# Optimization experiments

Measured on AMD Instinct MI355X. Metric: run time of the kernel, lower is better.

The kernel has to match this reference:

```python
import jax, jax.numpy as jnp
import numpy as np

N_HEAD = 16
N_KV_HEAD = 4
HEAD_DIM = 64  # n_embd // n_head = 1024 // 16
N_EMBD = 1024


def _alibi_bias(T, n_head, head_dim):
    # slopes: start = 2**(-2**(-(log2(H)-3))); slope_i = start**(i+1)
    start = 2.0 ** (-2.0 ** (-(np.log2(n_head) - 3.0)))
    slopes = jnp.asarray(start ** np.arange(1, n_head + 1), dtype=jnp.float32)  # [H]
    rel = (jnp.arange(T, dtype=jnp.float32)[None, :]
           - jnp.arange(T, dtype=jnp.float32)[:, None])  # [T,T], rel[i,j] = j - i
    bias = slopes[:, None, None] * rel[None, :, :]  # [H,T,T]
    # Faithful to the torch module: masked_fill(-inf) is then OVERWRITTEN by
    # torch.tril, which zeroes the upper triangle. Net effect: lower-tri alibi
    # values, 0 above the diagonal (NO causal masking).
    bias = jnp.tril(bias)
    return bias * (head_dim ** -0.5)  # extra scale applied in forward


def setup_inputs() -> dict:
    key = jax.random.key(0)
    ks = jax.random.split(key, 5)
    B, T, C = 4, 2048, N_EMBD
    w_scale = 0.02
    return {
        "x": jax.random.normal(ks[0], (B, T, C), dtype=jnp.float32),
        "Wq": jax.random.normal(ks[1], (C, C), dtype=jnp.float32) * w_scale,
        "Wkv": jax.random.normal(ks[2], (2 * N_KV_HEAD * HEAD_DIM, C), dtype=jnp.float32) * w_scale,
        "Wproj": jax.random.normal(ks[3], (C, C), dtype=jnp.float32) * w_scale,
        "bproj": jnp.zeros((C,), dtype=jnp.float32),
    }


def reference(x, Wq, Wkv, Wproj, bproj):
    B, T, C = x.shape
    H, KVH, D = N_HEAD, N_KV_HEAD, HEAD_DIM
    ratio = H // KVH

    q = jnp.einsum('btc,ec->bte', x, Wq).reshape(B, T, H, D).transpose(0, 2, 1, 3)  # [B,H,T,D]
    kv = jnp.einsum('btc,ec->bte', x, Wkv)  # [B,T,2*KVH*D]
    k, v = jnp.split(kv, 2, axis=-1)
    k = k.reshape(B, T, KVH, D).transpose(0, 2, 1, 3)  # [B,KVH,T,D]
    v = v.reshape(B, T, KVH, D).transpose(0, 2, 1, 3)
    # torch .repeat tiles whole blocks: query head h uses kv head h % KVH
    k = jnp.tile(k, (1, ratio, 1, 1))  # [B,H,T,D]
    v = jnp.tile(v, (1, ratio, 1, 1))

    bias = _alibi_bias(T, H, D)  # [H,T,T], already *= D**-0.5
    scores = jnp.einsum('bhtd,bhsd->bhts', q, k) * (D ** -0.5) + bias[None]
    attn = jax.nn.softmax(scores, axis=-1)
    out = jnp.einsum('bhts,bhsd->bhtd', attn, v)  # [B,H,T,D]
    out = out.transpose(0, 2, 1, 3).reshape(B, T, C)
    return jnp.einsum('btc,ec->bte', out, Wproj) + bproj
```

## Files before the change

### kernel.cpp

```cpp
#include <hip/hip_runtime.h>
#include <hip/hip_bf16.h>
#include <cstdint>

typedef __bf16 bf16;
typedef bf16 bf16x2 __attribute__((ext_vector_type(2)));
typedef bf16 bf16x4 __attribute__((ext_vector_type(4)));
typedef bf16 bf16x8 __attribute__((ext_vector_type(8)));
typedef float f32x4 __attribute__((ext_vector_type(4)));
typedef unsigned int uint32x2_t __attribute__((ext_vector_type(2)));
typedef unsigned int uint32x4_t __attribute__((ext_vector_type(4)));

#define MFMA16(a, b, c) __builtin_amdgcn_mfma_f32_16x16x32_bf16((a), (b), (c), 0, 0, 0)

#define QSCALE 0.18033688011112042f

__device__ inline void async16(const bf16* g, bf16* l) {
  __builtin_amdgcn_global_load_lds(
      (const __attribute__((address_space(1))) void*)g,
      (__attribute__((address_space(3))) void*)l, 16, 0, 0);
}

__global__ void cast_all(const float* __restrict__ x, const float* __restrict__ wq,
                         const float* __restrict__ wkv, const float* __restrict__ wp,
                         bf16* __restrict__ xb, bf16* __restrict__ w1b,
                         bf16* __restrict__ wpb) {
  const int i = blockIdx.x * blockDim.x + threadIdx.x;
  const float4* src;
  bf16x4* dst;
  int idx;
  if (i < 2097152) {
    src = (const float4*)x; dst = (bf16x4*)xb; idx = i;
  } else if (i < 2359296) {
    src = (const float4*)wq; dst = (bf16x4*)w1b; idx = i - 2097152;
  } else if (i < 2490368) {
    src = (const float4*)wkv; dst = (bf16x4*)(w1b + 1048576); idx = i - 2359296;
  } else {
    src = (const float4*)wp; dst = (bf16x4*)wpb; idx = i - 2490368;
  }
  const float4 v = src[idx];
  bf16x4 o;
  o.x = (bf16)v.x; o.y = (bf16)v.y; o.z = (bf16)v.z; o.w = (bf16)v.w;
  dst[idx] = o;
}

__global__ __launch_bounds__(256, 2)
void gemm_qkv(const bf16* __restrict__ A, const bf16* __restrict__ B,
              bf16* __restrict__ qb, bf16* __restrict__ kb, bf16* __restrict__ vb) {
  constexpr int K = 1024;
  __shared__ bf16 sA[128 * 64];
  __shared__ bf16 sB[128 * 64];
  const int tid = threadIdx.x;
  const int lane = tid & 63, wid = tid >> 6;
  const int col = lane & 15, quad = lane >> 4;
  const int wm = wid >> 1, wn = wid & 1;
  const int m0 = blockIdx.y * 128, n0 = blockIdx.x * 128;
  const int c7 = col & 7;

  f32x4 acc[4][4];
  const f32x4 z = {0.f, 0.f, 0.f, 0.f};
#pragma unroll
  for (int mi = 0; mi < 4; mi++)
#pragma unroll
    for (int ni = 0; ni < 4; ni++) acc[mi][ni] = z;

  for (int k0 = 0; k0 < K; k0 += 64) {
    __syncthreads();
#pragma unroll
    for (int c = 0; c < 4; ++c) {
      const int idx = c * 256 + tid;
      const int row = idx >> 3, kc = idx & 7;
      const int gkc = kc ^ (row & 7);
      async16(&A[(size_t)(m0 + row) * K + k0 + gkc * 8], &sA[idx * 8]);
      async16(&B[(size_t)(n0 + row) * K + k0 + gkc * 8], &sB[idx * 8]);
    }
    __syncthreads();
#pragma unroll
    for (int ks = 0; ks < 2; ++ks) {
      bf16x8 af[4], bfr[4];
#pragma unroll
      for (int i = 0; i < 4; i++)
        af[i] = *(const bf16x8*)&sA[(wm * 64 + i * 16 + col) * 64 +
                                    (((ks * 4 + quad) ^ c7) << 3)];
#pragma unroll
      for (int i = 0; i < 4; i++)
        bfr[i] = *(const bf16x8*)&sB[(wn * 64 + i * 16 + col) * 64 +
                                     (((ks * 4 + quad) ^ c7) << 3)];
#pragma unroll
      for (int mi = 0; mi < 4; mi++)
#pragma unroll
        for (int ni = 0; ni < 4; ni++)
          acc[mi][ni] = MFMA16(af[mi], bfr[ni], acc[mi][ni]);
    }
  }
#pragma unroll
  for (int mi = 0; mi < 4; mi++) {
#pragma unroll
    for (int ni = 0; ni < 4; ni++) {
      const int e = n0 + wn * 64 + ni * 16 + col;
#pragma unroll
      for (int r = 0; r < 4; r++) {
        const int m = m0 + wm * 64 + mi * 16 + quad * 4 + r;
        const int bb = m >> 11, t = m & 2047;
        if (e < 1024) {
          qb[(((size_t)bb * 16 + (e >> 6)) * 2048 + t) * 64 + (e & 63)] =
              (bf16)(acc[mi][ni][r] * QSCALE);
        } else if (e < 1280) {
          const int f = e - 1024;
          kb[(((size_t)bb * 4 + (f >> 6)) * 2048 + t) * 64 + (f & 63)] =
              (bf16)acc[mi][ni][r];
        } else {
          const int f = e - 1280;
          vb[(((size_t)bb * 4 + (f >> 6)) * 2048 + t) * 64 + (f & 63)] =
              (bf16)acc[mi][ni][r];
        }
      }
    }
  }
}

__global__ __launch_bounds__(256, 2)
void gemm_proj(const bf16* __restrict__ A, const bf16* __restrict__ B,
               const float* __restrict__ bias, float* __restrict__ out) {
  constexpr int K = 1024;
  __shared__ bf16 sA[128 * 64];
  __shared__ bf16 sB[128 * 64];
  const int tid = threadIdx.x;
  const int lane = tid & 63, wid = tid >> 6;
  const int col = lane & 15, quad = lane >> 4;
  const int wm = wid >> 1, wn = wid & 1;
  const int m0 = blockIdx.y * 128, n0 = blockIdx.x * 128;
  const int c7 = col & 7;

  f32x4 acc[4][4];
  const f32x4 z = {0.f, 0.f, 0.f, 0.f};
#pragma unroll
  for (int mi = 0; mi < 4; mi++)
#pragma unroll
    for (int ni = 0; ni < 4; ni++) acc[mi][ni] = z;

  for (int k0 = 0; k0 < K; k0 += 64) {
    __syncthreads();
#pragma unroll
    for (int c = 0; c < 4; ++c) {
      const int idx = c * 256 + tid;
      const int row = idx >> 3, kc = idx & 7;
      const int gkc = kc ^ (row & 7);
      async16(&A[(size_t)(m0 + row) * K + k0 + gkc * 8], &sA[idx * 8]);
      async16(&B[(size_t)(n0 + row) * K + k0 + gkc * 8], &sB[idx * 8]);
    }
    __syncthreads();
#pragma unroll
    for (int ks = 0; ks < 2; ++ks) {
      bf16x8 af[4], bfr[4];
#pragma unroll
      for (int i = 0; i < 4; i++)
        af[i] = *(const bf16x8*)&sA[(wm * 64 + i * 16 + col) * 64 +
                                    (((ks * 4 + quad) ^ c7) << 3)];
#pragma unroll
      for (int i = 0; i < 4; i++)
        bfr[i] = *(const bf16x8*)&sB[(wn * 64 + i * 16 + col) * 64 +
                                     (((ks * 4 + quad) ^ c7) << 3)];
#pragma unroll
      for (int mi = 0; mi < 4; mi++)
#pragma unroll
        for (int ni = 0; ni < 4; ni++)
          acc[mi][ni] = MFMA16(af[mi], bfr[ni], acc[mi][ni]);
    }
  }
#pragma unroll
  for (int mi = 0; mi < 4; mi++) {
#pragma unroll
    for (int ni = 0; ni < 4; ni++) {
      const int e = n0 + wn * 64 + ni * 16 + col;
      const float be = bias[e];
#pragma unroll
      for (int r = 0; r < 4; r++) {
        const int m = m0 + wm * 64 + mi * 16 + quad * 4 + r;
        out[(size_t)m * 1024 + e] = acc[mi][ni][r] + be;
      }
    }
  }
}

#define COMMIT_V(svc_)                                                      \
  _Pragma("unroll")                                                         \
  for (int j = 0; j < 8; j++) {                                             \
    bf16x2 pr; pr.x = vr0[j]; pr.y = vr1[j];                                \
    *(bf16x2*)&(svc_)[(kc * 8 + j) * 72 + ((blkv ^ kc) << 3) + rlv] = pr;   \
  }

#define QK_STRIP(Sx_, mb_)                                                  \
  {                                                                         \
    bf16x8 ak0[2], ak1[2];                                                  \
    _Pragma("unroll")                                                       \
    for (int t = 0; t < 2; t++) {                                           \
      ak0[t] = *(const bf16x8*)&skw[(((mb_) + t) * 16 + col) * 64 +         \
                                    ((quad ^ c7) << 3)];                    \
      ak1[t] = *(const bf16x8*)&skw[(((mb_) + t) * 16 + col) * 64 +         \
                                    (((4 + quad) ^ c7) << 3)];              \
    }                                                                       \
    __builtin_amdgcn_s_setprio(1);                                          \
    _Pragma("unroll")                                                       \
    for (int t = 0; t < 2; t++)                                             \
      _Pragma("unroll")                                                     \
      for (int ni = 0; ni < 4; ni++)                                        \
        Sx_[t][ni] = MFMA16(ak0[t], bq[ni][0], z);                          \
    _Pragma("unroll")                                                       \
    for (int t = 0; t < 2; t++)                                             \
      _Pragma("unroll")                                                     \
      for (int ni = 0; ni < 4; ni++)                                        \
        Sx_[t][ni] = MFMA16(ak1[t], bq[ni][1], Sx_[t][ni]);                 \
    __builtin_amdgcn_s_setprio(0);                                          \
  }

#define PV_KS(kspv_, svp_)                                                  \
  {                                                                         \
    bf16x8 bv[4];                                                           \
    _Pragma("unroll")                                                       \
    for (int nd = 0; nd < 4; nd++) {                                        \
      const int d = nd * 16 + col;                                          \
      bv[nd] = *(const bf16x8*)&(svp_)[d * 72 +                             \
                   ((((kspv_) * 4 + quad) ^ (d >> 3)) << 3)];               \
    }                                                                       \
    __builtin_amdgcn_s_setprio(1);                                          \
    _Pragma("unroll")                                                       \
    for (int mi = 0; mi < 4; mi++) {                                        \
      _Pragma("unroll")                                                     \
      for (int nd = 0; nd < 4; nd++)                                        \
        O[mi][nd] = MFMA16(ap[mi][kspv_], bv[nd], O[mi][nd]);               \
      Osum[mi] = MFMA16(ap[mi][kspv_], bones, Osum[mi]);                    \
    }                                                                       \
    __builtin_amdgcn_s_setprio(0);                                          \
  }

#define SM_STRIP(Sx_, mb_, kspv_)                                           \
  _Pragma("unroll")                                                         \
  for (int ni = 0; ni < 4; ni++) {                                          \
    unsigned plo[2], phi[2];                                                \
    _Pragma("unroll")                                                       \
    for (int t = 0; t < 2; t++) {                                           \
      const int U = c0 + ((mb_) + t) * 16 - qbase - ni * 16;                \
      f32x4 p;                                                              \
      if (U <= -15) {                                                       \
        const float bb = cb * (float)(U + qoff);                            \
        _Pragma("unroll")                                                   \
        for (int r = 0; r < 4; r++)                                         \
          p[r] = __builtin_amdgcn_exp2f(Sx_[t][ni][r] + (bb + cb * (float)r)); \
      } else if (U >= 16) {                                                 \
        _Pragma("unroll")                                                   \
        for (int r = 0; r < 4; r++)                                         \
          p[r] = __builtin_amdgcn_exp2f(Sx_[t][ni][r]);                     \
      } else {                                                              \
        const float relf = (float)(U + qoff);                               \
        _Pragma("unroll")                                                   \
        for (int r = 0; r < 4; r++) {                                       \
          const float rr = relf + (float)r;                                 \
          const float bb = (rr <= 0.f) ? cb * rr : 0.f;                     \
          p[r] = __builtin_amdgcn_exp2f(Sx_[t][ni][r] + bb);                \
        }                                                                   \
      }                                                                     \
      bf16x2 lo, hi;                                                        \
      lo.x = (bf16)p[0]; lo.y = (bf16)p[1];                                 \
      hi.x = (bf16)p[2]; hi.y = (bf16)p[3];                                 \
      plo[t] = __builtin_bit_cast(unsigned, lo);                            \
      phi[t] = __builtin_bit_cast(unsigned, hi);                            \
    }                                                                       \
    uint32x2_t rl = __builtin_amdgcn_permlane32_swap(plo[0], plo[1], false, false); \
    uint32x2_t rh = __builtin_amdgcn_permlane32_swap(phi[0], phi[1], false, false); \
    uint32x2_t w02 = __builtin_amdgcn_permlane16_swap(rl.x, rl.y, false, false);    \
    uint32x2_t w13 = __builtin_amdgcn_permlane16_swap(rh.x, rh.y, false, false);    \
    uint32x4_t W;                                                           \
    W.x = w02.x; W.y = w13.x; W.z = w02.y; W.w = w13.y;                     \
    ap[ni][kspv_] = __builtin_bit_cast(bf16x8, W);                          \
  }

__global__ __launch_bounds__(256, 2)
void attn_alibi(const bf16* __restrict__ qb, const bf16* __restrict__ kb,
                const bf16* __restrict__ vb, bf16* __restrict__ ob) {
  __shared__ bf16 sK[2][64 * 64];
  __shared__ bf16 sVt[3][64 * 72];
  const int tid = threadIdx.x;
  const int lane = tid & 63, wid = tid >> 6;
  const int col = lane & 15, quad = lane >> 4;
  const int c7 = col & 7;
  const int bh = blockIdx.y;
  const int b = bh >> 4, h = bh & 15, kvh = h & 3;
  const int qbase = __builtin_amdgcn_readfirstlane(blockIdx.x * 256 + wid * 64);

  const bf16* qptr = qb + ((size_t)(b * 16 + h) * 2048 + qbase) * 64;
  const bf16* kptr = kb + ((size_t)(b * 4 + kvh) * 2048) * 64;
  const bf16* vptr = vb + ((size_t)(b * 4 + kvh) * 2048) * 64;

  bf16x8 bq[4][2];
#pragma unroll
  for (int ni = 0; ni < 4; ni++)
#pragma unroll
    for (int ks = 0; ks < 2; ks++)
      bq[ni][ks] = *(const bf16x8*)&qptr[(ni * 16 + col) * 64 + ks * 32 + quad * 8];

  bf16x8 bones;
#pragma unroll
  for (int j = 0; j < 8; j++) bones[j] = (bf16)1.0f;

  f32x4 O[4][4];
  f32x4 Osum[4];
  const f32x4 z = {0.f, 0.f, 0.f, 0.f};
#pragma unroll
  for (int mi = 0; mi < 4; mi++) {
    Osum[mi] = z;
#pragma unroll
    for (int nd = 0; nd < 4; nd++) O[mi][nd] = z;
  }

  const float cb = exp2f(-0.5f * (float)(h + 1)) * QSCALE;
  const int qoff = quad * 4 - col;

  const int rowA = tid >> 3, kc = tid & 7;
  const int kxA = (kc ^ (rowA & 7)) << 3;
  const int rv = rowA * 2;
  const int blkv = rv >> 3, rlv = rv & 7;

  async16(&kptr[(size_t)rowA * 64 + kxA], &sK[0][tid * 8]);
  async16(&kptr[(size_t)(rowA + 32) * 64 + kxA], &sK[0][(256 + tid) * 8]);
  bf16x8 vr0 = *(const bf16x8*)&vptr[(size_t)rv * 64 + kc * 8];
  bf16x8 vr1 = *(const bf16x8*)&vptr[(size_t)(rv + 1) * 64 + kc * 8];

  bf16x8 ap[4][2];

  {
    const int c0 = 0;
    COMMIT_V(sVt[0]);
    __syncthreads();
    async16(&kptr[(size_t)(64 + rowA) * 64 + kxA], &sK[1][tid * 8]);
    async16(&kptr[(size_t)(64 + rowA + 32) * 64 + kxA], &sK[1][(256 + tid) * 8]);
    vr0 = *(const bf16x8*)&vptr[(size_t)(64 + rv) * 64 + kc * 8];
    vr1 = *(const bf16x8*)&vptr[(size_t)(64 + rv + 1) * 64 + kc * 8];

    const bf16* skw = sK[0];
    f32x4 Sa[2][4], Sb[2][4];
    QK_STRIP(Sa, 0);
    SM_STRIP(Sa, 0, 0);
    QK_STRIP(Sb, 2);
    SM_STRIP(Sb, 2, 1);
  }

  int bufi = 1, ivc = 1, ivp = 0;
  for (int c0 = 64; c0 < 2048; c0 += 64) {
    const bf16* skw = sK[bufi];
    const bf16* svp = sVt[ivp];
    COMMIT_V(sVt[ivc]);
    __syncthreads();

    {
      const int cn = (c0 + 64 < 2048) ? c0 + 64 : 0;
      bf16* skn = sK[bufi ^ 1];
      async16(&kptr[(size_t)(cn + rowA) * 64 + kxA], &skn[tid * 8]);
      async16(&kptr[(size_t)(cn + rowA + 32) * 64 + kxA], &skn[(256 + tid) * 8]);
      vr0 = *(const bf16x8*)&vptr[(size_t)(cn + rv) * 64 + kc * 8];
      vr1 = *(const bf16x8*)&vptr[(size_t)(cn + rv + 1) * 64 + kc * 8];
    }

    f32x4 Sa[2][4], Sb[2][4];
    QK_STRIP(Sa, 0);
    PV_KS(0, svp);
    SM_STRIP(Sa, 0, 0);
    QK_STRIP(Sb, 2);
    PV_KS(1, svp);
    SM_STRIP(Sb, 2, 1);

    bufi ^= 1;
    ivp = ivc;
    ivc = (ivc == 2) ? 0 : ivc + 1;
  }

  {
    const bf16* svp = sVt[ivp];
    PV_KS(0, svp);
    PV_KS(1, svp);
  }

#pragma unroll
  for (int mi = 0; mi < 4; mi++) {
#pragma unroll
    for (int r = 0; r < 4; r++) {
      const float inv = 1.0f / Osum[mi][r];
      const int t = qbase + mi * 16 + quad * 4 + r;
#pragma unroll
      for (int nd = 0; nd < 4; nd++) {
        ob[((size_t)b * 2048 + t) * 1024 + h * 64 + nd * 16 + col] =
            (bf16)(O[mi][nd][r] * inv);
      }
    }
  }
}

extern "C" void kernel_launch(void* const* d_in, const int* in_sizes, int n_in,
                              void* d_out, int out_size, void* d_ws, size_t ws_size,
                              hipStream_t stream) {
  const float* x     = (const float*)d_in[0];
  const float* Wq    = (const float*)d_in[1];
  const float* Wkv   = (const float*)d_in[2];
  const float* Wproj = (const float*)d_in[3];
  const float* bproj = (const float*)d_in[4];
  float* out = (float*)d_out;

  bf16* xb  = (bf16*)d_ws;
  bf16* w1b = xb  + 8388608;
  bf16* wpb = w1b + 1572864;
  bf16* qb  = wpb + 1048576;
  bf16* kb  = qb  + 8388608;
  bf16* vb  = kb  + 2097152;
  bf16* aob = vb  + 2097152;

  cast_all<<<10752, 256, 0, stream>>>(x, Wq, Wkv, Wproj, xb, w1b, wpb);
  gemm_qkv<<<dim3(12, 64), 256, 0, stream>>>(xb, w1b, qb, kb, vb);
  attn_alibi<<<dim3(8, 64), 256, 0, stream>>>(qb, kb, vb, aob);
  gemm_proj<<<dim3(8, 64), 256, 0, stream>>>(aob, wpb, bproj, out);
}
```

Before: 239.7 us.

## Process 128-key tiles per barrier in attention and swizzle GEMM block order

The attention kernel now loads 128 keys per iteration into double-buffered K and V tiles, which halves the number of barriers per sequence. It drops the previous software pipeline, where the PV step of the last tile overlapped the QK step of the current one, in favour of a simpler in-order QK, softmax and PV sequence for each 64-key sub-tile. Both GEMMs also remap block indices with an XOR-style grouping, aiming for better L2 reuse. The trade-offs are more LDS per block, which may cut occupancy, and less overlap between MFMA and softmax work.

```diff
diff --git a/kernel.cpp b/kernel.cpp
--- a/kernel.cpp
+++ b/kernel.cpp
@@ -47,13 +47,16 @@
 void gemm_qkv(const bf16* __restrict__ A, const bf16* __restrict__ B,
               bf16* __restrict__ qb, bf16* __restrict__ kb, bf16* __restrict__ vb) {
   constexpr int K = 1024;
+  constexpr int NX = 12;
   __shared__ bf16 sA[128 * 64];
   __shared__ bf16 sB[128 * 64];
   const int tid = threadIdx.x;
   const int lane = tid & 63, wid = tid >> 6;
   const int col = lane & 15, quad = lane >> 4;
   const int wm = wid >> 1, wn = wid & 1;
-  const int m0 = blockIdx.y * 128, n0 = blockIdx.x * 128;
+  const int bid = blockIdx.y * NX + blockIdx.x;
+  const int swz = (bid & 7) * (NX * 64 / 8) + (bid >> 3);
+  const int m0 = (swz / NX) * 128, n0 = (swz % NX) * 128;
   const int c7 = col & 7;
 
   f32x4 acc[4][4];
@@ -122,13 +125,16 @@
 void gemm_proj(const bf16* __restrict__ A, const bf16* __restrict__ B,
                const float* __restrict__ bias, float* __restrict__ out) {
   constexpr int K = 1024;
+  constexpr int NX = 8;
   __shared__ bf16 sA[128 * 64];
   __shared__ bf16 sB[128 * 64];
   const int tid = threadIdx.x;
   const int lane = tid & 63, wid = tid >> 6;
   const int col = lane & 15, quad = lane >> 4;
   const int wm = wid >> 1, wn = wid & 1;
-  const int m0 = blockIdx.y * 128, n0 = blockIdx.x * 128;
+  const int bid = blockIdx.y * NX + blockIdx.x;
+  const int swz = (bid & 7) * (NX * 64 / 8) + (bid >> 3);
+  const int m0 = (swz / NX) * 128, n0 = (swz % NX) * 128;
   const int c7 = col & 7;
 
   f32x4 acc[4][4];
@@ -182,81 +188,31 @@
   }
 }
 
-#define COMMIT_V(svc_)                                                      \
-  _Pragma("unroll")                                                         \
-  for (int j = 0; j < 8; j++) {                                             \
-    bf16x2 pr; pr.x = vr0[j]; pr.y = vr1[j];                                \
-    *(bf16x2*)&(svc_)[(kc * 8 + j) * 72 + ((blkv ^ kc) << 3) + rlv] = pr;   \
-  }
-
-#define QK_STRIP(Sx_, mb_)                                                  \
-  {                                                                         \
-    bf16x8 ak0[2], ak1[2];                                                  \
-    _Pragma("unroll")                                                       \
-    for (int t = 0; t < 2; t++) {                                           \
-      ak0[t] = *(const bf16x8*)&skw[(((mb_) + t) * 16 + col) * 64 +         \
-                                    ((quad ^ c7) << 3)];                    \
-      ak1[t] = *(const bf16x8*)&skw[(((mb_) + t) * 16 + col) * 64 +         \
-                                    (((4 + quad) ^ c7) << 3)];              \
-    }                                                                       \
-    __builtin_amdgcn_s_setprio(1);                                          \
-    _Pragma("unroll")                                                       \
-    for (int t = 0; t < 2; t++)                                             \
-      _Pragma("unroll")                                                     \
-      for (int ni = 0; ni < 4; ni++)                                        \
-        Sx_[t][ni] = MFMA16(ak0[t], bq[ni][0], z);                          \
-    _Pragma("unroll")                                                       \
-    for (int t = 0; t < 2; t++)                                             \
-      _Pragma("unroll")                                                     \
-      for (int ni = 0; ni < 4; ni++)                                        \
-        Sx_[t][ni] = MFMA16(ak1[t], bq[ni][1], Sx_[t][ni]);                 \
-    __builtin_amdgcn_s_setprio(0);                                          \
-  }
-
-#define PV_KS(kspv_, svp_)                                                  \
-  {                                                                         \
-    bf16x8 bv[4];                                                           \
-    _Pragma("unroll")                                                       \
-    for (int nd = 0; nd < 4; nd++) {                                        \
-      const int d = nd * 16 + col;                                          \
-      bv[nd] = *(const bf16x8*)&(svp_)[d * 72 +                             \
-                   ((((kspv_) * 4 + quad) ^ (d >> 3)) << 3)];               \
-    }                                                                       \
-    __builtin_amdgcn_s_setprio(1);                                          \
-    _Pragma("unroll")                                                       \
-    for (int mi = 0; mi < 4; mi++) {                                        \
-      _Pragma("unroll")                                                     \
-      for (int nd = 0; nd < 4; nd++)                                        \
-        O[mi][nd] = MFMA16(ap[mi][kspv_], bv[nd], O[mi][nd]);               \
-      Osum[mi] = MFMA16(ap[mi][kspv_], bones, Osum[mi]);                    \
-    }                                                                       \
-    __builtin_amdgcn_s_setprio(0);                                          \
-  }
-
-#define SM_STRIP(Sx_, mb_, kspv_)                                           \
+#define SM_HALF(kp_)                                                        \
   _Pragma("unroll")                                                         \
   for (int ni = 0; ni < 4; ni++) {                                          \
     unsigned plo[2], phi[2];                                                \
     _Pragma("unroll")                                                       \
     for (int t = 0; t < 2; t++) {                                           \
-      const int U = c0 + ((mb_) + t) * 16 - qbase - ni * 16;                \
+      const int mi = (kp_) * 2 + t;                                         \
+      const int U = c0s + mi * 16 - qbase - ni * 16;                        \
       f32x4 p;                                                              \
       if (U <= -15) {                                                       \
         const float bb = cb * (float)(U + qoff);                            \
         _Pragma("unroll")                                                   \
         for (int r = 0; r < 4; r++)                                         \
-          p[r] = __builtin_amdgcn_exp2f(Sx_[t][ni][r] + (bb + cb * (float)r)); \
+          p[r] = __builtin_amdgcn_exp2f(S[mi][ni][r] + (bb + cb * (float)r)); \
       } else if (U >= 16) {                                                 \
         _Pragma("unroll")                                                   \
         for (int r = 0; r < 4; r++)                                         \
-          p[r] = __builtin_amdgcn_exp2f(Sx_[t][ni][r]);                     \
+          p[r] = __builtin_amdgcn_exp2f(S[mi][ni][r]);                      \
       } else {                                                              \
         const float relf = (float)(U + qoff);                               \
         _Pragma("unroll")                                                   \
         for (int r = 0; r < 4; r++) {                                       \
           const float rr = relf + (float)r;                                 \
           const float bb = (rr <= 0.f) ? cb * rr : 0.f;                     \
-          p[r] = __builtin_amdgcn_exp2f(Sx_[t][ni][r] + bb);                \
+          p[r] = __builtin_amdgcn_exp2f(S[mi][ni][r] + bb);                 \
         }                                                                   \
       }                                                                     \
       bf16x2 lo, hi;                                                        \
@@ -271,14 +227,34 @@
     uint32x2_t w13 = __builtin_amdgcn_permlane16_swap(rh.x, rh.y, false, false);    \
     uint32x4_t W;                                                           \
     W.x = w02.x; W.y = w13.x; W.z = w02.y; W.w = w13.y;                     \
-    ap[ni][kspv_] = __builtin_bit_cast(bf16x8, W);                          \
+    ap[ni][kp_] = __builtin_bit_cast(bf16x8, W);                            \
+  }
+
+#define PV_HALF(kp_)                                                        \
+  {                                                                         \
+    bf16x8 bv[4];                                                           \
+    _Pragma("unroll")                                                       \
+    for (int nd = 0; nd < 4; nd++) {                                        \
+      const int d = nd * 16 + col;                                          \
+      bv[nd] = *(const bf16x8*)&svw[d * 136 + rbase +                       \
+                   ((((kp_) * 4 + quad) ^ (d >> 3)) << 3)];                 \
+    }                                                                       \
+    __builtin_amdgcn_s_setprio(1);                                          \
+    _Pragma("unroll")                                                       \
+    for (int mi = 0; mi < 4; mi++) {                                        \
+      _Pragma("unroll")                                                     \
+      for (int nd = 0; nd < 4; nd++)                                        \
+        O[mi][nd] = MFMA16(ap[mi][kp_], bv[nd], O[mi][nd]);                 \
+      Osum[mi] = MFMA16(ap[mi][kp_], bones, Osum[mi]);                      \
+    }                                                                       \
+    __builtin_amdgcn_s_setprio(0);                                          \
   }
 
 __global__ __launch_bounds__(256, 2)
 void attn_alibi(const bf16* __restrict__ qb, const bf16* __restrict__ kb,
                 const bf16* __restrict__ vb, bf16* __restrict__ ob) {
-  __shared__ bf16 sK[2][64 * 64];
-  __shared__ bf16 sVt[3][64 * 72];
+  __shared__ bf16 sK[2][128 * 64];
+  __shared__ bf16 sVt[2][64 * 136];
   const int tid = threadIdx.x;
   const int lane = tid & 63, wid = tid >> 6;
   const int col = lane & 15, quad = lane >> 4;
@@ -320,63 +296,83 @@
   const int rv = rowA * 2;
   const int blkv = rv >> 3, rlv = rv & 7;
 
-  async16(&kptr[(size_t)rowA * 64 + kxA], &sK[0][tid * 8]);
+  async16(&kptr[(size_t)(rowA) * 64 + kxA], &sK[0][tid * 8]);
   async16(&kptr[(size_t)(rowA + 32) * 64 + kxA], &sK[0][(256 + tid) * 8]);
-  bf16x8 vr0 = *(const bf16x8*)&vptr[(size_t)rv * 64 + kc * 8];
-  bf16x8 vr1 = *(const bf16x8*)&vptr[(size_t)(rv + 1) * 64 + kc * 8];
-
-  bf16x8 ap[4][2];
-
-  {
-    const int c0 = 0;
-    COMMIT_V(sVt[0]);
+  async16(&kptr[(size_t)(rowA + 64) * 64 + kxA], &sK[0][(512 + tid) * 8]);
+  async16(&kptr[(size_t)(rowA + 96) * 64 + kxA], &sK[0][(768 + tid) * 8]);
+  bf16x8 vrA0 = *(const bf16x8*)&vptr[(size_t)rv * 64 + kc * 8];
+  bf16x8 vrA1 = *(const bf16x8*)&vptr[(size_t)(rv + 1) * 64 + kc * 8];
+  bf16x8 vrB0 = *(const bf16x8*)&vptr[(size_t)(64 + rv) * 64 + kc * 8];
+  bf16x8 vrB1 = *(const bf16x8*)&vptr[(size_t)(64 + rv + 1) * 64 + kc * 8];
+
+  int bufi = 0;
+  for (int c0 = 0; c0 < 2048; c0 += 128, bufi ^= 1) {
+    bf16* skw = sK[bufi];
+    bf16* svw = sVt[bufi];
+#pragma unroll
+    for (int j = 0; j < 8; j++) {
+      bf16x2 pa;
+      pa.x = vrA0[j];
+      pa.y = vrA1[j];
+      *(bf16x2*)&svw[(kc * 8 + j) * 136 + ((blkv ^ kc) << 3) + rlv] = pa;
+      bf16x2 pb;
+      pb.x = vrB0[j];
+      pb.y = vrB1[j];
+      *(bf16x2*)&svw[(kc * 8 + j) * 136 + 64 + ((blkv ^ kc) << 3) + rlv] = pb;
+    }
     __syncthreads();
-    async16(&kptr[(size_t)(64 + rowA) * 64 + kxA], &sK[1][tid * 8]);
-    async16(&kptr[(size_t)(64 + rowA + 32) * 64 + kxA], &sK[1][(256 + tid) * 8]);
-    vr0 = *(const bf16x8*)&vptr[(size_t)(64 + rv) * 64 + kc * 8];
-    vr1 = *(const bf16x8*)&vptr[(size_t)(64 + rv + 1) * 64 + kc * 8];
-
-    const bf16* skw = sK[0];
-    f32x4 Sa[2][4], Sb[2][4];
-    QK_STRIP(Sa, 0);
-    SM_STRIP(Sa, 0, 0);
-    QK_STRIP(Sb, 2);
-    SM_STRIP(Sb, 2, 1);
-  }
-
-  int bufi = 1, ivc = 1, ivp = 0;
-  for (int c0 = 64; c0 < 2048; c0 += 64) {
-    const bf16* skw = sK[bufi];
-    const bf16* svp = sVt[ivp];
-    COMMIT_V(sVt[ivc]);
-    __syncthreads();
 
     {
-      const int cn = (c0 + 64 < 2048) ? c0 + 64 : 0;
+      const int cn = (c0 + 128 < 2048) ? c0 + 128 : 0;
       bf16* skn = sK[bufi ^ 1];
       async16(&kptr[(size_t)(cn + rowA) * 64 + kxA], &skn[tid * 8]);
       async16(&kptr[(size_t)(cn + rowA + 32) * 64 + kxA], &skn[(256 + tid) * 8]);
-      vr0 = *(const bf16x8*)&vptr[(size_t)(cn + rv) * 64 + kc * 8];
-      vr1 = *(const bf16x8*)&vptr[(size_t)(cn + rv + 1) * 64 + kc * 8];
-    }
-
-    f32x4 Sa[2][4], Sb[2][4];
-    QK_STRIP(Sa, 0);
-    PV_KS(0, svp);
-    SM_STRIP(Sa, 0, 0);
-    QK_STRIP(Sb, 2);
-    PV_KS(1, svp);
-    SM_STRIP(Sb, 2, 1);
-
-    bufi ^= 1;
-    ivp = ivc;
-    ivc = (ivc == 2) ? 0 : ivc + 1;
-  }
-
-  {
-    const bf16* svp = sVt[ivp];
-    PV_KS(0, svp);
-    PV_KS(1, svp);
+      async16(&kptr[(size_t)(cn + rowA + 64) * 64 + kxA], &skn[(512 + tid) * 8]);
+      async16(&kptr[(size_t)(cn + rowA + 96) * 64 + kxA], &skn[(768 + tid) * 8]);
+      vrA0 = *(const bf16x8*)&vptr[(size_t)(cn + rv) * 64 + kc * 8];
+      vrA1 = *(const bf16x8*)&vptr[(size_t)(cn + rv + 1) * 64 + kc * 8];
+      vrB0 = *(const bf16x8*)&vptr[(size_t)(cn + 64 + rv) * 64 + kc * 8];
+      vrB1 = *(const bf16x8*)&vptr[(size_t)(cn + 64 + rv + 1) * 64 + kc * 8];
+    }
+
+#pragma unroll
+    for (int sub = 0; sub < 2; sub++) {
+      const int rbase = sub * 64;
+      const int c0s = c0 + rbase;
+
+      f32x4 S[4][4];
+      {
+        bf16x8 ak[4];
+#pragma unroll
+        for (int mi = 0; mi < 4; mi++)
+          ak[mi] = *(const bf16x8*)&skw[(rbase + mi * 16 + col) * 64 +
+                                        ((quad ^ c7) << 3)];
+        __builtin_amdgcn_s_setprio(1);
+#pragma unroll
+        for (int mi = 0; mi < 4; mi++)
+#pragma unroll
+          for (int ni = 0; ni < 4; ni++)
+            S[mi][ni] = MFMA16(ak[mi], bq[ni][0], z);
+        __builtin_amdgcn_s_setprio(0);
+#pragma unroll
+        for (int mi = 0; mi < 4; mi++)
+          ak[mi] = *(const bf16x8*)&skw[(rbase + mi * 16 + col) * 64 +
+                                        (((4 + quad) ^ c7) << 3)];
+        __builtin_amdgcn_s_setprio(1);
+#pragma unroll
+        for (int mi = 0; mi < 4; mi++)
+#pragma unroll
+          for (int ni = 0; ni < 4; ni++)
+            S[mi][ni] = MFMA16(ak[mi], bq[ni][1], S[mi][ni]);
+        __builtin_amdgcn_s_setprio(0);
+      }
+
+      bf16x8 ap[4][2];
+      SM_HALF(0);
+      PV_HALF(0);
+      SM_HALF(1);
+      PV_HALF(1);
+    }
   }
 
 #pragma unroll
```

Measured after the change: 258.9 us. 1.08x slower.
